# Optimization experiments

Hardware: AMD Instinct MI355X
Metric: run time of the kernel (lower is better)

The kernel has to match this reference:

```python
import jax, jax.numpy as jnp
import numpy as np

N = 8192      # total packed vision tokens
D = 1280      # hidden_size
H = 16        # num_heads
K = 80        # head_dim = D // H
M = 16        # number of image segments
LMAX = 1024   # static upper bound on per-image segment length
SCALE = K ** (-0.5)
NEG = -1e30   # finite mask value (avoids NaN on fully-padded rows)


def _rotate_half(x):
    h = x.shape[-1] // 2
    return jnp.concatenate([-x[..., h:], x[..., :h]], axis=-1)


def setup_inputs() -> dict:
    key = jax.random.key(0)
    ks = jax.random.split(key, 5)
    hidden = jax.random.normal(ks[0], (N, D), jnp.float32)
    # ragged per-image lengths (sum == N, each <= LMAX)
    lengths = np.array([256, 768] * (M // 2), dtype=np.int32)
    cu = jnp.asarray(np.concatenate([[0], np.cumsum(lengths)]).astype(np.int32))
    # rotary tables, shape (N, head_dim)
    inv_freq = 1.0 / (10000.0 ** (np.arange(0, K, 2, dtype=np.float32) / K))  # (K/2,)
    freqs = np.arange(N, dtype=np.float32)[:, None] * inv_freq[None, :]       # (N, K/2)
    emb = np.concatenate([freqs, freqs], axis=-1)                              # (N, K)
    cos = jnp.asarray(np.cos(emb), jnp.float32)
    sin = jnp.asarray(np.sin(emb), jnp.float32)
    W_qkv = jax.random.normal(ks[1], (D, 3 * D), jnp.float32) * (D ** -0.5)
    b_qkv = jax.random.normal(ks[2], (3 * D,), jnp.float32) * 0.01
    W_proj = jax.random.normal(ks[3], (D, D), jnp.float32) * (D ** -0.5)
    b_proj = jax.random.normal(ks[4], (D,), jnp.float32) * 0.01
    return dict(hidden_ND=hidden, cu_seqlens=cu, cos_NK=cos, sin_NK=sin,
                W_qkv=W_qkv, b_qkv=b_qkv, W_proj=W_proj, b_proj=b_proj)


def reference(hidden_ND, cu_seqlens, cos_NK, sin_NK, W_qkv, b_qkv, W_proj, b_proj):
    n = hidden_ND.shape[0]
    # fused QKV projection
    qkv = (hidden_ND @ W_qkv + b_qkv).reshape(n, 3, H, K)
    q, k, v = qkv[:, 0], qkv[:, 1], qkv[:, 2]          # (N, H, K)
    # inline RoPE on Q/K (fp32 math, as in apply_rotary_pos_emb_vision)
    cos = cos_NK[:, None, :]
    sin = sin_NK[:, None, :]
    q = q * cos + _rotate_half(q) * sin
    k = k * cos + _rotate_half(k) * sin
    # gather packed tokens into padded per-segment blocks (honors segment sparsity:
    # no cross-segment tiles are ever materialized)
    lengths = jnp.diff(cu_seqlens)                                  # (M,)
    idx = cu_seqlens[:-1, None] + jnp.arange(LMAX)[None, :]         # (M, LMAX)
    valid = jnp.arange(LMAX)[None, :] < lengths[:, None]            # (M, LMAX)
    idxc = jnp.minimum(idx, n - 1)
    qg, kg, vg = q[idxc], k[idxc], v[idxc]                          # (M, LMAX, H, K)
    # per-segment attention
    scores = jnp.einsum('mqhd,mkhd->mhqk', qg, kg) * SCALE          # (M, H, LMAX, LMAX)
    mask = valid[:, None, :, None] & valid[:, None, None, :]
    scores = jnp.where(mask, scores, NEG)
    p = jax.nn.softmax(scores, axis=-1)
    og = jnp.einsum('mhqk,mkhd->mqhd', p, vg)                       # (M, LMAX, H, K)
    # scatter back to packed layout: token n -> (segment, position)
    seg = jnp.searchsorted(cu_seqlens[1:], jnp.arange(n), side='right')
    pos = jnp.arange(n) - cu_seqlens[seg]
    attn_ND = og[seg, pos].reshape(n, H * K)
    return attn_ND @ W_proj + b_proj
```

## Files before the change

kernel.cpp:

```cpp
#include <hip/hip_runtime.h>
#include <hip/hip_bf16.h>
#include <stdint.h>

#define NTOK 8192
#define DMODEL 1280
#define NHEAD 16
#define HDIM 80
#define NSEG 16
#define SCALE_F 0.11180339887498949f
#define NEG_F -1e30f

typedef __bf16 bf16x8 __attribute__((ext_vector_type(8)));
typedef float f32x4 __attribute__((ext_vector_type(4)));

__device__ __forceinline__ void gload_lds16(const void* g, void* l) {
  __builtin_amdgcn_global_load_lds((__attribute__((address_space(1))) void*)g,
                                   (__attribute__((address_space(3))) void*)l,
                                   16, 0, 0);
}

__global__ __launch_bounds__(256)
void cvt_f32_to_bf16(const float* __restrict__ src, __hip_bfloat16* __restrict__ dst) {
  int i = (blockIdx.x * 256 + threadIdx.x) * 4;
  float4 v = *(const float4*)(src + i);
  __align__(8) __hip_bfloat16 o[4] = {__float2bfloat16(v.x), __float2bfloat16(v.y),
                                      __float2bfloat16(v.z), __float2bfloat16(v.w)};
  *(uint2*)(dst + i) = *(const uint2*)o;
}

__global__ __launch_bounds__(256)
void transpose_w(const float* __restrict__ src, __hip_bfloat16* __restrict__ dst,
                 int R, int C) {
  __shared__ __hip_bfloat16 tile[32][33];
  int c0 = blockIdx.x * 32, r0 = blockIdx.y * 32;
  int tx = threadIdx.x & 31, ty = threadIdx.x >> 5;
#pragma unroll
  for (int i = 0; i < 4; ++i) {
    int r = ty + i * 8;
    tile[r][tx] = __float2bfloat16(src[(size_t)(r0 + r) * C + c0 + tx]);
  }
  __syncthreads();
#pragma unroll
  for (int i = 0; i < 4; ++i) {
    int r = ty + i * 8;
    dst[(size_t)(c0 + r) * R + r0 + tx] = tile[tx][r];
  }
}

__global__ __launch_bounds__(256)
void rope2(__hip_bfloat16* __restrict__ qkv,
           const float* __restrict__ cosb, const float* __restrict__ sinb) {
  int t = blockIdx.x * 256 + threadIdx.x;
  int p = t % 5;
  int rest = t / 5;
  int h = rest & 15;
  int qk = (rest >> 4) & 1;
  int n = rest >> 5;
  size_t base = (size_t)n * 3840 + qk * 1280 + h * 80 + p * 8;
  const float* cb = cosb + n * 80 + p * 8;
  const float* sb = sinb + n * 80 + p * 8;
  float4 cA = *(const float4*)cb, cB = *(const float4*)(cb + 4);
  float4 cC = *(const float4*)(cb + 40), cD = *(const float4*)(cb + 44);
  float4 sA = *(const float4*)sb, sB = *(const float4*)(sb + 4);
  float4 sC = *(const float4*)(sb + 40), sD = *(const float4*)(sb + 44);
  float c0[8] = {cA.x, cA.y, cA.z, cA.w, cB.x, cB.y, cB.z, cB.w};
  float c1[8] = {cC.x, cC.y, cC.z, cC.w, cD.x, cD.y, cD.z, cD.w};
  float s0[8] = {sA.x, sA.y, sA.z, sA.w, sB.x, sB.y, sB.z, sB.w};
  float s1[8] = {sC.x, sC.y, sC.z, sC.w, sD.x, sD.y, sD.z, sD.w};
  uint4 lou = *(const uint4*)(qkv + base);
  uint4 hiu = *(const uint4*)(qkv + base + 40);
  __align__(16) __hip_bfloat16 lo[8], hh[8], olo[8], ohi[8];
  *(uint4*)lo = lou; *(uint4*)hh = hiu;
#pragma unroll
  for (int e = 0; e < 8; ++e) {
    float x0 = __bfloat162float(lo[e]);
    float x1 = __bfloat162float(hh[e]);
    olo[e] = __float2bfloat16(x0 * c0[e] - x1 * s0[e]);
    ohi[e] = __float2bfloat16(x1 * c1[e] + x0 * s1[e]);
  }
  *(uint4*)(qkv + base) = *(const uint4*)olo;
  *(uint4*)(qkv + base + 40) = *(const uint4*)ohi;
}

template <bool OUT_F32, bool A_F32>
__global__ __launch_bounds__(256)
void gemm128(const void* __restrict__ Av, int lda,
             const __hip_bfloat16* __restrict__ Bt,
             const float* __restrict__ bias,
             void* __restrict__ Cv, int M, int N, int K) {
  __shared__ __align__(16) __hip_bfloat16 lds[8192];
  const int tid = threadIdx.x;
  const int lane = tid & 63;
  const int wave = tid >> 6;
  const int wr = wave >> 1, wc = wave & 1;
  const int lr = lane & 15;
  const int hi = lane >> 4;
  const int sw = (lr >> 1) & 3;
  const int lk = (hi ^ sw) << 3;
  const int m0 = blockIdx.x * 128;
  const int n0 = blockIdx.y * 128;

  f32x4 zero = {0.f, 0.f, 0.f, 0.f};
  f32x4 acc[4][4];
#pragma unroll
  for (int i = 0; i < 4; ++i)
#pragma unroll
    for (int j = 0; j < 4; ++j) acc[i][j] = zero;

  for (int k0 = 0; k0 < K; k0 += 32) {
#pragma unroll
    for (int j = 0; j < 2; ++j) {
      int v = j * 256 + tid;
      int row = v >> 2;
      int cb = ((v & 3) ^ ((v >> 3) & 3)) << 3;
      gload_lds16(Bt + (size_t)(n0 + row) * K + k0 + cb,
                  &lds[4096 + wave * 512 + j * 2048]);
    }
    if constexpr (A_F32) {
      const float* A32 = (const float*)Av;
      float4 vv[4];
#pragma unroll
      for (int j = 0; j < 4; ++j) {
        int task = j * 256 + tid;
        int row = task >> 3, cc = task & 7;
        vv[j] = *(const float4*)(A32 + (size_t)(m0 + row) * lda + k0 + cc * 4);
      }
#pragma unroll
      for (int j = 0; j < 4; ++j) {
        int task = j * 256 + tid;
        int row = task >> 3, cc = task & 7;
        int s = (cc >> 1) ^ ((row >> 1) & 3);
        __align__(8) __hip_bfloat16 t[4] = {
            __float2bfloat16(vv[j].x), __float2bfloat16(vv[j].y),
            __float2bfloat16(vv[j].z), __float2bfloat16(vv[j].w)};
        *(uint2*)&lds[row * 32 + s * 8 + (cc & 1) * 4] = *(const uint2*)t;
      }
    } else {
      const __hip_bfloat16* Abf = (const __hip_bfloat16*)Av;
#pragma unroll
      for (int j = 0; j < 2; ++j) {
        int v = j * 256 + tid;
        int row = v >> 2;
        int cb = ((v & 3) ^ ((v >> 3) & 3)) << 3;
        gload_lds16(Abf + (size_t)(m0 + row) * lda + k0 + cb,
                    &lds[wave * 512 + j * 2048]);
      }
    }
    __syncthreads();

    bf16x8 af[4], bfr[4];
#pragma unroll
    for (int i = 0; i < 4; ++i) {
      af[i]  = *(const bf16x8*)&lds[(wr * 64 + i * 16 + lr) * 32 + lk];
      bfr[i] = *(const bf16x8*)&lds[4096 + (wc * 64 + i * 16 + lr) * 32 + lk];
    }
#pragma unroll
    for (int i = 0; i < 4; ++i)
#pragma unroll
      for (int j = 0; j < 4; ++j)
        acc[i][j] = __builtin_amdgcn_mfma_f32_16x16x32_bf16(af[i], bfr[j], acc[i][j], 0, 0, 0);
    __syncthreads();
  }

  const int r0 = (lane >> 4) << 2;
#pragma unroll
  for (int j = 0; j < 4; ++j) {
    int col = n0 + wc * 64 + j * 16 + lr;
    float bv = bias[col];
#pragma unroll
    for (int i = 0; i < 4; ++i) {
      int rowb = m0 + wr * 64 + i * 16 + r0;
#pragma unroll
      for (int r = 0; r < 4; ++r) {
        float val = acc[i][j][r] + bv;
        if (OUT_F32)
          ((float*)Cv)[(size_t)(rowb + r) * N + col] = val;
        else
          ((__hip_bfloat16*)Cv)[(size_t)(rowb + r) * N + col] = __float2bfloat16(val);
      }
    }
  }
}

template <bool OUT_F32>
__global__ __launch_bounds__(512, 4)
void gemm256(const __hip_bfloat16* __restrict__ A, int lda,
             const __hip_bfloat16* __restrict__ Bt,
             const float* __restrict__ bias,
             void* __restrict__ Cv, int M, int N, int K) {
  __shared__ __align__(16) __hip_bfloat16 lds[2][12288];
  const int tid = threadIdx.x;
  const int lane = tid & 63;
  const int wave = tid >> 6;
  const int wr = wave >> 1;
  const int wc = wave & 1;
  const int lr = lane & 15;
  const int hi = lane >> 4;
  const int lk = (hi ^ ((lr >> 1) & 3)) << 3;
  const int m0 = blockIdx.x * 256;
  const int n0 = blockIdx.y * 128;

  const int scol = ((tid & 3) ^ ((tid >> 3) & 3)) * 8;
  const __hip_bfloat16* srcA = A + (size_t)(m0 + (tid >> 2)) * lda + scol;
  const __hip_bfloat16* srcB = Bt + (size_t)(n0 + (tid >> 2)) * K + scol;
  const size_t rowA128 = (size_t)128 * lda;

  auto stage = [&](int kt, int b) {
    const __hip_bfloat16* sa = srcA + kt * 32;
    gload_lds16(sa,           &lds[b][tid * 8]);
    gload_lds16(sa + rowA128, &lds[b][4096 + tid * 8]);
    gload_lds16(srcB + kt * 32, &lds[b][8192 + tid * 8]);
  };

  f32x4 acc[4][4];
  f32x4 fz = {0.f, 0.f, 0.f, 0.f};
#pragma unroll
  for (int i = 0; i < 4; ++i)
#pragma unroll
    for (int j = 0; j < 4; ++j) acc[i][j] = fz;

  const int nkt = K >> 5;
  stage(0, 0);
  asm volatile("s_waitcnt vmcnt(0)" ::: "memory");
  __builtin_amdgcn_sched_barrier(0);
  __builtin_amdgcn_s_barrier();

  for (int t = 0; t < nkt; ++t) {
    const int b = t & 1;
    const int ktn = (t + 1 < nkt) ? t + 1 : nkt - 1;
    const __hip_bfloat16* Ab = &lds[b][(wr * 64) * 32];
    const __hip_bfloat16* Bb = &lds[b][8192 + (wc * 64) * 32];

    bf16x8 af[4], bf[4];
#pragma unroll
    for (int i = 0; i < 4; ++i) af[i] = *(const bf16x8*)&Ab[(i * 16 + lr) * 32 + lk];
#pragma unroll
    for (int j = 0; j < 4; ++j) bf[j] = *(const bf16x8*)&Bb[(j * 16 + lr) * 32 + lk];
    stage(ktn, b ^ 1);
    __builtin_amdgcn_sched_barrier(0);
    __builtin_amdgcn_s_barrier();
    asm volatile("s_waitcnt lgkmcnt(0)" ::: "memory");
    __builtin_amdgcn_sched_barrier(0);
    __builtin_amdgcn_s_setprio(1);
#pragma unroll
    for (int i = 0; i < 4; ++i)
#pragma unroll
      for (int j = 0; j < 4; ++j)
        acc[i][j] = __builtin_amdgcn_mfma_f32_16x16x32_bf16(af[i], bf[j], acc[i][j], 0, 0, 0);
    __builtin_amdgcn_s_setprio(0);
    __builtin_amdgcn_sched_barrier(0);
    asm volatile("s_waitcnt vmcnt(0)" ::: "memory");
    __builtin_amdgcn_sched_barrier(0);
    __builtin_amdgcn_s_barrier();
  }

#pragma unroll
  for (int j = 0; j < 4; ++j) {
    int col = n0 + wc * 64 + j * 16 + lr;
    float bv = bias[col];
#pragma unroll
    for (int i = 0; i < 4; ++i) {
      int row0 = m0 + wr * 64 + i * 16 + hi * 4;
#pragma unroll
      for (int r = 0; r < 4; ++r) {
        float val = acc[i][j][r] + bv;
        if (OUT_F32)
          ((float*)Cv)[(size_t)(row0 + r) * N + col] = val;
        else
          ((__hip_bfloat16*)Cv)[(size_t)(row0 + r) * N + col] = __float2bfloat16(val);
      }
    }
  }
}

__global__ __launch_bounds__(256, 3)
void attn_fwd(__hip_bfloat16* __restrict__ qkv, const int* __restrict__ cu) {
  const int bid = blockIdx.x;
  const int l = (bid & 7) * 288 + (bid >> 3);
  const int h = l / 144;
  const int pid = l - h * 144;
  int seg = -1, qt = 0, start = 0, L = 0;
  int accq = 0;
#pragma unroll 1
  for (int s2 = 0; s2 < NSEG; ++s2) {
    int st = cu[s2], en = cu[s2 + 1];
    int len = en - st;
    int nq = (len + 63) >> 6;
    if (seg < 0 && pid < accq + nq) { seg = s2; qt = pid - accq; start = st; L = len; }
    accq += nq;
  }
  if (seg < 0) return;

  __shared__ __align__(16) __hip_bfloat16 Ks[2][64 * 80];
  __shared__ __align__(16) __hip_bfloat16 Vs[2][80 * 72];
  __shared__ __align__(16) __hip_bfloat16 Ps[4][16 * 72];

  const int tid = threadIdx.x;
  const int lane = tid & 63;
  const int wave = tid >> 6;
  const int lr = lane & 15;
  const int hi = lane >> 4;
  const int lk = hi * 8;
  const int nt = (L + 63) >> 6;

  bf16x8 aq[3];
  {
    bf16x8 z;
#pragma unroll
    for (int e = 0; e < 8; ++e) z[e] = (__bf16)0.0f;
    int qr = qt * 64 + wave * 16 + lr;
    if (qr > L - 1) qr = L - 1;
    const __hip_bfloat16* qp = qkv + (size_t)(start + qr) * 3840 + h * 80;
    bf16x8 a0 = *(const bf16x8*)(qp + lk);
    bf16x8 a1 = *(const bf16x8*)(qp + 32 + lk);
    bf16x8 a2 = (hi < 2) ? *(const bf16x8*)(qp + 64 + lk) : z;
#pragma unroll
    for (int e = 0; e < 8; ++e) {
      a0[e] = (__bf16)((float)a0[e] * SCALE_F);
      a1[e] = (__bf16)((float)a1[e] * SCALE_F);
      a2[e] = (__bf16)((float)a2[e] * SCALE_F);
    }
    aq[0] = a0; aq[1] = a1; aq[2] = a2;
  }

  const __hip_bfloat16* kbase = qkv + (size_t)start * 3840 + 1280 + h * 80;
  const __hip_bfloat16* vbase = qkv + (size_t)start * 3840 + 2560 + h * 80;

  auto stageK = [&](int t, int buf) {
#pragma unroll
    for (int j = 0; j < 3; ++j) {
      int i = wave + 4 * j;
      if (i < 10) {
        int E = i * 512 + lane * 8;
        int r = E / 80;
        int c = E - r * 80;
        int g = t * 64 + r;
        if (g > L - 1) g = L - 1;
        gload_lds16(kbase + (size_t)g * 3840 + c, (char*)&Ks[buf][0] + i * 1024);
      }
    }
  };
  uint4 vr[3];
  auto loadV = [&](int t) {
    int g = t * 64 + lane;
    if (g > L - 1) g = L - 1;
    size_t roff = (size_t)g * 3840;
#pragma unroll
    for (int j = 0; j < 3; ++j) {
      int c = wave + 4 * j;
      if (c < 10) vr[j] = *(const uint4*)(vbase + roff + c * 8);
    }
  };
  auto writeV = [&](int buf) {
#pragma unroll
    for (int j = 0; j < 3; ++j) {
      int c = wave + 4 * j;
      if (c < 10) {
        __align__(16) __hip_bfloat16 tmp[8];
        *(uint4*)tmp = vr[j];
#pragma unroll
        for (int e = 0; e < 8; ++e) Vs[buf][(c * 8 + e) * 72 + lane] = tmp[e];
      }
    }
  };

  float m_run[4], l_part[4];
  f32x4 fz = {0.f, 0.f, 0.f, 0.f};
  f32x4 accO[5];
#pragma unroll
  for (int r = 0; r < 4; ++r) { m_run[r] = NEG_F; l_part[r] = 0.f; }
#pragma unroll
  for (int d = 0; d < 5; ++d) accO[d] = fz;

  stageK(0, 0);
  loadV(0);
  writeV(0);
  loadV(nt > 1 ? 1 : 0);
  __syncthreads();

  int cur = 0;
  for (int t = 0; t < nt; ++t) {
    const bool more = (t + 1 < nt);
    if (more) {
      stageK(t + 1, cur ^ 1);
      writeV(cur ^ 1);
      loadV(t + 2 < nt ? t + 2 : nt - 1);
    }

    f32x4 s[4] = {fz, fz, fz, fz};
#pragma unroll
    for (int ks = 0; ks < 3; ++ks) {
#pragma unroll
      for (int j = 0; j < 4; ++j) {
        bf16x8 bk = *(const bf16x8*)&Ks[cur][(j * 16 + lr) * 80 + ks * 32 + lk];
        s[j] = __builtin_amdgcn_mfma_f32_16x16x32_bf16(aq[ks], bk, s[j], 0, 0, 0);
      }
    }
    if (t * 64 + 64 > L) {
#pragma unroll
      for (int j = 0; j < 4; ++j) {
        bool vj = (t * 64 + j * 16 + lr) < L;
#pragma unroll
        for (int r = 0; r < 4; ++r)
          s[j][r] = vj ? s[j][r] : NEG_F;
      }
    }
    float mx[4];
    bool need = false;
#pragma unroll
    for (int r = 0; r < 4; ++r) {
      mx[r] = fmaxf(fmaxf(s[0][r], s[1][r]), fmaxf(s[2][r], s[3][r]));
      need |= mx[r] > m_run[r] + 8.0f;
    }
    if (__any(need)) {
#pragma unroll
      for (int off = 1; off < 16; off <<= 1)
#pragma unroll
        for (int r = 0; r < 4; ++r)
          mx[r] = fmaxf(mx[r], __shfl_xor(mx[r], off, 64));
#pragma unroll
      for (int r = 0; r < 4; ++r) {
        float mn = fmaxf(m_run[r], mx[r]);
        float sf = __expf(m_run[r] - mn);
        m_run[r] = mn;
        l_part[r] *= sf;
#pragma unroll
        for (int d = 0; d < 5; ++d) accO[d][r] *= sf;
      }
    }
#pragma unroll
    for (int r = 0; r < 4; ++r) {
      float a0 = __expf(s[0][r] - m_run[r]); s[0][r] = a0;
      float a1 = __expf(s[1][r] - m_run[r]); s[1][r] = a1;
      float a2 = __expf(s[2][r] - m_run[r]); s[2][r] = a2;
      float a3 = __expf(s[3][r] - m_run[r]); s[3][r] = a3;
      l_part[r] += (a0 + a1) + (a2 + a3);
    }

    __hip_bfloat16* pw = &Ps[wave][0];
#pragma unroll
    for (int j = 0; j < 4; ++j)
#pragma unroll
      for (int r = 0; r < 4; ++r)
        pw[(hi * 4 + r) * 72 + j * 16 + lr] = __float2bfloat16(s[j][r]);
    asm volatile("s_waitcnt lgkmcnt(0)" ::: "memory");
    __builtin_amdgcn_sched_barrier(0);
    bf16x8 ap0 = *(const bf16x8*)&pw[lr * 72 + lk];
    bf16x8 ap1 = *(const bf16x8*)&pw[lr * 72 + 32 + lk];
#pragma unroll
    for (int d = 0; d < 5; ++d) {
      bf16x8 bv0 = *(const bf16x8*)&Vs[cur][(d * 16 + lr) * 72 + lk];
      bf16x8 bv1 = *(const bf16x8*)&Vs[cur][(d * 16 + lr) * 72 + 32 + lk];
      accO[d] = __builtin_amdgcn_mfma_f32_16x16x32_bf16(ap0, bv0, accO[d], 0, 0, 0);
      accO[d] = __builtin_amdgcn_mfma_f32_16x16x32_bf16(ap1, bv1, accO[d], 0, 0, 0);
    }

    __syncthreads();
    cur ^= 1;
  }

#pragma unroll
  for (int off = 1; off < 16; off <<= 1)
#pragma unroll
    for (int r = 0; r < 4; ++r)
      l_part[r] += __shfl_xor(l_part[r], off, 64);
  float rl[4];
#pragma unroll
  for (int r = 0; r < 4; ++r) rl[r] = 1.0f / l_part[r];
#pragma unroll
  for (int d = 0; d < 5; ++d)
#pragma unroll
    for (int r = 0; r < 4; ++r) {
      int row = qt * 64 + wave * 16 + hi * 4 + r;
      if (row < L)
        qkv[(size_t)(start + row) * 3840 + h * 80 + d * 16 + lr] =
            __float2bfloat16(accO[d][r] * rl[r]);
    }
}

extern "C" void kernel_launch(void* const* d_in, const int* in_sizes, int n_in,
                              void* d_out, int out_size, void* d_ws, size_t ws_size,
                              hipStream_t stream) {
  const float* hidden = (const float*)d_in[0];
  const int*   cu     = (const int*)d_in[1];
  const float* cosb   = (const float*)d_in[2];
  const float* sinb   = (const float*)d_in[3];
  const float* Wqkv   = (const float*)d_in[4];
  const float* bqkv   = (const float*)d_in[5];
  const float* Wproj  = (const float*)d_in[6];
  const float* bproj  = (const float*)d_in[7];
  float* out = (float*)d_out;
  char* ws = (char*)d_ws;

  __hip_bfloat16* qkv    = (__hip_bfloat16*)(ws);
  __hip_bfloat16* wqkvT  = (__hip_bfloat16*)(ws + 62914560);
  __hip_bfloat16* wprojT = (__hip_bfloat16*)(ws + 72744960);
  __hip_bfloat16* hbf    = (__hip_bfloat16*)(ws + 76021760);
  const bool use_hbf = ws_size >= (size_t)96993280;

  transpose_w<<<dim3(120, 40), 256, 0, stream>>>(Wqkv, wqkvT, 1280, 3840);
  transpose_w<<<dim3(40, 40), 256, 0, stream>>>(Wproj, wprojT, 1280, 1280);
  if (use_hbf) {
    cvt_f32_to_bf16<<<10240, 256, 0, stream>>>(hidden, hbf);
    gemm256<false><<<dim3(32, 30), 512, 0, stream>>>(hbf, 1280, wqkvT, bqkv, qkv, 8192, 3840, 1280);
  } else {
    gemm128<false, true><<<dim3(64, 30), 256, 0, stream>>>(hidden, 1280, wqkvT, bqkv, qkv, 8192, 3840, 1280);
  }
  rope2<<<5120, 256, 0, stream>>>(qkv, cosb, sinb);
  attn_fwd<<<2304, 256, 0, stream>>>(qkv, cu);
  gemm256<true><<<dim3(32, 10), 512, 0, stream>>>(qkv, 3840, wprojT, bproj, out, 8192, 1280, 1280);
}
```

Baseline: 246.4 us.

## Process two 16-row Q fragments per wave to double K/V tile reuse

Each attention block now covers 128 query rows instead of 64, with every wave holding two Q fragments and separate softmax/accumulator state for each. Every K/V tile staged in shared memory is therefore reused for twice as many queries, halving K/V global loads and staging work, and the grid shrinks from 2304 to 1024 blocks. The cost is more registers per thread, which may lower occupancy under launch_bounds(256,3), fewer blocks to fill the device, and more wasted padded rows for 256- and 768-length segments. The P tile in shared memory is reused serially for the two fragments.

```diff
diff --git a/kernel.cpp b/kernel.cpp
--- a/kernel.cpp
+++ b/kernel.cpp
@@ -276,16 +276,16 @@
 __global__ __launch_bounds__(256, 3)
 void attn_fwd(__hip_bfloat16* __restrict__ qkv, const int* __restrict__ cu) {
   const int bid = blockIdx.x;
-  const int l = (bid & 7) * 288 + (bid >> 3);
-  const int h = l / 144;
-  const int pid = l - h * 144;
+  const int l = (bid & 7) * 128 + (bid >> 3);
+  const int h = l >> 6;
+  const int pid = l & 63;
   int seg = -1, qt = 0, start = 0, L = 0;
   int accq = 0;
 #pragma unroll 1
   for (int s2 = 0; s2 < NSEG; ++s2) {
     int st = cu[s2], en = cu[s2 + 1];
     int len = en - st;
-    int nq = (len + 63) >> 6;
+    int nq = (len + 127) >> 7;
     if (seg < 0 && pid < accq + nq) { seg = s2; qt = pid - accq; start = st; L = len; }
     accq += nq;
   }
@@ -303,24 +303,27 @@
   const int lk = hi * 8;
   const int nt = (L + 63) >> 6;
 
-  bf16x8 aq[3];
+  bf16x8 aq[2][3];
   {
     bf16x8 z;
 #pragma unroll
     for (int e = 0; e < 8; ++e) z[e] = (__bf16)0.0f;
-    int qr = qt * 64 + wave * 16 + lr;
-    if (qr > L - 1) qr = L - 1;
-    const __hip_bfloat16* qp = qkv + (size_t)(start + qr) * 3840 + h * 80;
-    bf16x8 a0 = *(const bf16x8*)(qp + lk);
-    bf16x8 a1 = *(const bf16x8*)(qp + 32 + lk);
-    bf16x8 a2 = (hi < 2) ? *(const bf16x8*)(qp + 64 + lk) : z;
-#pragma unroll
-    for (int e = 0; e < 8; ++e) {
-      a0[e] = (__bf16)((float)a0[e] * SCALE_F);
-      a1[e] = (__bf16)((float)a1[e] * SCALE_F);
-      a2[e] = (__bf16)((float)a2[e] * SCALE_F);
-    }
-    aq[0] = a0; aq[1] = a1; aq[2] = a2;
+#pragma unroll
+    for (int f = 0; f < 2; ++f) {
+      int qr = qt * 128 + wave * 32 + f * 16 + lr;
+      if (qr > L - 1) qr = L - 1;
+      const __hip_bfloat16* qp = qkv + (size_t)(start + qr) * 3840 + h * 80;
+      bf16x8 a0 = *(const bf16x8*)(qp + lk);
+      bf16x8 a1 = *(const bf16x8*)(qp + 32 + lk);
+      bf16x8 a2 = (hi < 2) ? *(const bf16x8*)(qp + 64 + lk) : z;
+#pragma unroll
+      for (int e = 0; e < 8; ++e) {
+        a0[e] = (__bf16)((float)a0[e] * SCALE_F);
+        a1[e] = (__bf16)((float)a1[e] * SCALE_F);
+        a2[e] = (__bf16)((float)a2[e] * SCALE_F);
+      }
+      aq[f][0] = a0; aq[f][1] = a1; aq[f][2] = a2;
+    }
   }
 
   const __hip_bfloat16* kbase = qkv + (size_t)start * 3840 + 1280 + h * 80;
@@ -364,13 +367,16 @@
     }
   };
 
-  float m_run[4], l_part[4];
+  float m_run[2][4], l_part[2][4];
   f32x4 fz = {0.f, 0.f, 0.f, 0.f};
-  f32x4 accO[5];
-#pragma unroll
-  for (int r = 0; r < 4; ++r) { m_run[r] = NEG_F; l_part[r] = 0.f; }
-#pragma unroll
-  for (int d = 0; d < 5; ++d) accO[d] = fz;
+  f32x4 accO[2][5];
+#pragma unroll
+  for (int f = 0; f < 2; ++f) {
+#pragma unroll
+    for (int r = 0; r < 4; ++r) { m_run[f][r] = NEG_F; l_part[f][r] = 0.f; }
+#pragma unroll
+    for (int d = 0; d < 5; ++d) accO[f][d] = fz;
+  }
 
   stageK(0, 0);
   loadV(0);
@@ -387,13 +393,18 @@
       loadV(t + 2 < nt ? t + 2 : nt - 1);
     }
 
-    f32x4 s[4] = {fz, fz, fz, fz};
+    f32x4 s[2][4];
+#pragma unroll
+    for (int f = 0; f < 2; ++f)
+#pragma unroll
+      for (int j = 0; j < 4; ++j) s[f][j] = fz;
 #pragma unroll
     for (int ks = 0; ks < 3; ++ks) {
 #pragma unroll
       for (int j = 0; j < 4; ++j) {
         bf16x8 bk = *(const bf16x8*)&Ks[cur][(j * 16 + lr) * 80 + ks * 32 + lk];
-        s[j] = __builtin_amdgcn_mfma_f32_16x16x32_bf16(aq[ks], bk, s[j], 0, 0, 0);
+        s[0][j] = __builtin_amdgcn_mfma_f32_16x16x32_bf16(aq[0][ks], bk, s[0][j], 0, 0, 0);
+        s[1][j] = __builtin_amdgcn_mfma_f32_16x16x32_bf16(aq[1][ks], bk, s[1][j], 0, 0, 0);
       }
     }
     if (t * 64 + 64 > L) {
@@ -401,58 +412,73 @@
       for (int j = 0; j < 4; ++j) {
         bool vj = (t * 64 + j * 16 + lr) < L;
 #pragma unroll
+        for (int f = 0; f < 2; ++f)
+#pragma unroll
+          for (int r = 0; r < 4; ++r)
+            s[f][j][r] = vj ? s[f][j][r] : NEG_F;
+      }
+    }
+    float mx[2][4];
+    bool need = false;
+#pragma unroll
+    for (int f = 0; f < 2; ++f)
+#pragma unroll
+      for (int r = 0; r < 4; ++r) {
+        mx[f][r] = fmaxf(fmaxf(s[f][0][r], s[f][1][r]), fmaxf(s[f][2][r], s[f][3][r]));
+        need |= mx[f][r] > m_run[f][r] + 8.0f;
+      }
+    if (__any(need)) {
+#pragma unroll
+      for (int off = 1; off < 16; off <<= 1)
+#pragma unroll
+        for (int f = 0; f < 2; ++f)
+#pragma unroll
+          for (int r = 0; r < 4; ++r)
+            mx[f][r] = fmaxf(mx[f][r], __shfl_xor(mx[f][r], off, 64));
+#pragma unroll
+      for (int f = 0; f < 2; ++f)
+#pragma unroll
+        for (int r = 0; r < 4; ++r) {
+          float mn = fmaxf(m_run[f][r], mx[f][r]);
+          float sf = __expf(m_run[f][r] - mn);
+          m_run[f][r] = mn;
+          l_part[f][r] *= sf;
+#pragma unroll
+          for (int d = 0; d < 5; ++d) accO[f][d][r] *= sf;
+        }
+    }
+#pragma unroll
+    for (int f = 0; f < 2; ++f)
+#pragma unroll
+      for (int r = 0; r < 4; ++r) {
+        float a0 = __expf(s[f][0][r] - m_run[f][r]); s[f][0][r] = a0;
+        float a1 = __expf(s[f][1][r] - m_run[f][r]); s[f][1][r] = a1;
+        float a2 = __expf(s[f][2][r] - m_run[f][r]); s[f][2][r] = a2;
+        float a3 = __expf(s[f][3][r] - m_run[f][r]); s[f][3][r] = a3;
+        l_part[f][r] += (a0 + a1) + (a2 + a3);
+      }
+
+    __hip_bfloat16* pw = &Ps[wave][0];
+#pragma unroll
+    for (int f = 0; f < 2; ++f) {
+#pragma unroll
+      for (int j = 0; j < 4; ++j)
+#pragma unroll
         for (int r = 0; r < 4; ++r)
-          s[j][r] = vj ? s[j][r] : NEG_F;
-      }
-    }
-    float mx[4];
-    bool need = false;
-#pragma unroll
-    for (int r = 0; r < 4; ++r) {
-      mx[r] = fmaxf(fmaxf(s[0][r], s[1][r]), fmaxf(s[2][r], s[3][r]));
-      need |= mx[r] > m_run[r] + 8.0f;
-    }
-    if (__any(need)) {
-#pragma unroll
-      for (int off = 1; off < 16; off <<= 1)
-#pragma unroll
-        for (int r = 0; r < 4; ++r)
-          mx[r] = fmaxf(mx[r], __shfl_xor(mx[r], off, 64));
-#pragma unroll
-      for (int r = 0; r < 4; ++r) {
-        float mn = fmaxf(m_run[r], mx[r]);
-        float sf = __expf(m_run[r] - mn);
-        m_run[r] = mn;
-        l_part[r] *= sf;
-#pragma unroll
-        for (int d = 0; d < 5; ++d) accO[d][r] *= sf;
-      }
-    }
-#pragma unroll
-    for (int r = 0; r < 4; ++r) {
-      float a0 = __expf(s[0][r] - m_run[r]); s[0][r] = a0;
-      float a1 = __expf(s[1][r] - m_run[r]); s[1][r] = a1;
-      float a2 = __expf(s[2][r] - m_run[r]); s[2][r] = a2;
-      float a3 = __expf(s[3][r] - m_run[r]); s[3][r] = a3;
-      l_part[r] += (a0 + a1) + (a2 + a3);
-    }
-
-    __hip_bfloat16* pw = &Ps[wave][0];
-#pragma unroll
-    for (int j = 0; j < 4; ++j)
-#pragma unroll
-      for (int r = 0; r < 4; ++r)
-        pw[(hi * 4 + r) * 72 + j * 16 + lr] = __float2bfloat16(s[j][r]);
-    asm volatile("s_waitcnt lgkmcnt(0)" ::: "memory");
-    __builtin_amdgcn_sched_barrier(0);
-    bf16x8 ap0 = *(const bf16x8*)&pw[lr * 72 + lk];
-    bf16x8 ap1 = *(const bf16x8*)&pw[lr * 72 + 32 + lk];
-#pragma unroll
-    for (int d = 0; d < 5; ++d) {
-      bf16x8 bv0 = *(const bf16x8*)&Vs[cur][(d * 16 + lr) * 72 + lk];
-      bf16x8 bv1 = *(const bf16x8*)&Vs[cur][(d * 16 + lr) * 72 + 32 + lk];
-      accO[d] = __builtin_amdgcn_mfma_f32_16x16x32_bf16(ap0, bv0, accO[d], 0, 0, 0);
-      accO[d] = __builtin_amdgcn_mfma_f32_16x16x32_bf16(ap1, bv1, accO[d], 0, 0, 0);
+          pw[(hi * 4 + r) * 72 + j * 16 + lr] = __float2bfloat16(s[f][j][r]);
+      asm volatile("s_waitcnt lgkmcnt(0)" ::: "memory");
+      __builtin_amdgcn_sched_barrier(0);
+      bf16x8 ap0 = *(const bf16x8*)&pw[lr * 72 + lk];
+      bf16x8 ap1 = *(const bf16x8*)&pw[lr * 72 + 32 + lk];
+      asm volatile("s_waitcnt lgkmcnt(0)" ::: "memory");
+      __builtin_amdgcn_sched_barrier(0);
+#pragma unroll
+      for (int d = 0; d < 5; ++d) {
+        bf16x8 bv0 = *(const bf16x8*)&Vs[cur][(d * 16 + lr) * 72 + lk];
+        bf16x8 bv1 = *(const bf16x8*)&Vs[cur][(d * 16 + lr) * 72 + 32 + lk];
+        accO[f][d] = __builtin_amdgcn_mfma_f32_16x16x32_bf16(ap0, bv0, accO[f][d], 0, 0, 0);
+        accO[f][d] = __builtin_amdgcn_mfma_f32_16x16x32_bf16(ap1, bv1, accO[f][d], 0, 0, 0);
+      }
     }
 
     __syncthreads();
@@ -462,20 +488,25 @@
 #pragma unroll
   for (int off = 1; off < 16; off <<= 1)
 #pragma unroll
-    for (int r = 0; r < 4; ++r)
-      l_part[r] += __shfl_xor(l_part[r], off, 64);
-  float rl[4];
-#pragma unroll
-  for (int r = 0; r < 4; ++r) rl[r] = 1.0f / l_part[r];
-#pragma unroll
-  for (int d = 0; d < 5; ++d)
-#pragma unroll
-    for (int r = 0; r < 4; ++r) {
-      int row = qt * 64 + wave * 16 + hi * 4 + r;
-      if (row < L)
-        qkv[(size_t)(start + row) * 3840 + h * 80 + d * 16 + lr] =
-            __float2bfloat16(accO[d][r] * rl[r]);
-    }
+    for (int f = 0; f < 2; ++f)
+#pragma unroll
+      for (int r = 0; r < 4; ++r)
+        l_part[f][r] += __shfl_xor(l_part[f][r], off, 64);
+#pragma unroll
+  for (int f = 0; f < 2; ++f) {
+    float rl[4];
+#pragma unroll
+    for (int r = 0; r < 4; ++r) rl[r] = 1.0f / l_part[f][r];
+#pragma unroll
+    for (int d = 0; d < 5; ++d)
+#pragma unroll
+      for (int r = 0; r < 4; ++r) {
+        int row = qt * 128 + wave * 32 + f * 16 + hi * 4 + r;
+        if (row < L)
+          qkv[(size_t)(start + row) * 3840 + h * 80 + d * 16 + lr] =
+              __float2bfloat16(accO[f][d][r] * rl[r]);
+      }
+  }
 }
 
 extern "C" void kernel_launch(void* const* d_in, const int* in_sizes, int n_in,
@@ -507,6 +538,6 @@
     gemm128<false, true><<<dim3(64, 30), 256, 0, stream>>>(hidden, 1280, wqkvT, bqkv, qkv, 8192, 3840, 1280);
   }
   rope2<<<5120, 256, 0, stream>>>(qkv, cosb, sinb);
-  attn_fwd<<<2304, 256, 0, stream>>>(qkv, cu);
+  attn_fwd<<<1024, 256, 0, stream>>>(qkv, cu);
   gemm256<true><<<dim3(32, 10), 512, 0, stream>>>(qkv, 3840, wprojT, bproj, out, 8192, 1280, 1280);
 }
```

Result: no change. 245.4 us (-0.4%).
